# Kernel optimization log

Measured on AMD Instinct MI355X. Metric: run time of the kernel, lower is better.

Reference implementation:

```python
import jax, jax.numpy as jnp
import numpy as np

B, NPG, IN_DIM, H, E = 128, 500, 3, 128, 512000
N = B * NPG
NEG = -1e9  # stands in for -inf masked fill; exp underflows to exactly 0 in fp32
BN_EPS = 1e-5


def setup_inputs() -> dict:
    key = jax.random.key(0)
    ks = jax.random.split(key, 40)
    rn = lambda k, shape: (jax.random.normal(k, shape, jnp.float32) * 0.05)
    x = jax.random.normal(ks[0], (N, IN_DIM), jnp.float32)
    g = jax.random.randint(ks[1], (E,), 0, B)
    src = jax.random.randint(ks[2], (E,), 0, NPG) + g * NPG
    dst = jax.random.randint(ks[3], (E,), 0, NPG) + g * NPG
    edge_index = jnp.stack([src, dst]).astype(jnp.int32)
    batch = (jnp.arange(N) // NPG).astype(jnp.int32)
    feasible_mask = jax.random.uniform(ks[4], (B, NPG, NPG)) < 0.1
    feasible_mask = feasible_mask.at[:, 0, 0].set(True)  # >=1 feasible action/graph
    return dict(
        x=x, edge_index=edge_index, batch=batch, feasible_mask=feasible_mask,
        gin_W1_0=rn(ks[5], (IN_DIM, H)), gin_b1_0=jnp.zeros((H,), jnp.float32),
        gin_g_0=jnp.ones((H,), jnp.float32), gin_be_0=jnp.zeros((H,), jnp.float32),
        gin_W2_0=rn(ks[6], (H, H)), gin_b2_0=jnp.zeros((H,), jnp.float32),
        gin_W1=rn(ks[7], (3, H, H)), gin_b1=jnp.zeros((3, H), jnp.float32),
        gin_g=jnp.ones((3, H), jnp.float32), gin_be=jnp.zeros((3, H), jnp.float32),
        gin_W2=rn(ks[8], (3, H, H)), gin_b2=jnp.zeros((3, H), jnp.float32),
        pol_W1_0=rn(ks[9], (2 * H, H)), pol_b1_0=jnp.zeros((H,), jnp.float32),
        pol_W2_0=rn(ks[10], (H, H)), pol_b2_0=jnp.zeros((H,), jnp.float32),
        pol_W1=rn(ks[11], (2, H, H)), pol_b1=jnp.zeros((2, H), jnp.float32),
        pol_W2=rn(ks[12], (2, H, H)), pol_b2=jnp.zeros((2, H), jnp.float32),
    )


def _gin_conv(h, src, dst, deg, W1, b1, g, be, W2, b2):
    # mean-aggregate neighbors (self loops already in edge list), eps=0
    agg = jax.ops.segment_sum(h[src], dst, num_segments=N) / deg[:, None]
    z = (h + agg) @ W1 + b1
    mu = jnp.mean(z, axis=0)
    var = jnp.var(z, axis=0)  # biased var, as torch BN training mode
    z = (z - mu) * jax.lax.rsqrt(var + BN_EPS) * g + be
    return jax.nn.relu(z) @ W2 + b2


def reference(x, edge_index, batch, feasible_mask,
              gin_W1_0, gin_b1_0, gin_g_0, gin_be_0, gin_W2_0, gin_b2_0,
              gin_W1, gin_b1, gin_g, gin_be, gin_W2, gin_b2,
              pol_W1_0, pol_b1_0, pol_W2_0, pol_b2_0,
              pol_W1, pol_b1, pol_W2, pol_b2):
    # add self loops
    loop = jnp.arange(N, dtype=edge_index.dtype)
    src = jnp.concatenate([edge_index[0], loop])
    dst = jnp.concatenate([edge_index[1], loop])
    deg = jnp.maximum(jax.ops.segment_sum(jnp.ones_like(src, jnp.float32), dst, num_segments=N), 1.0)

    h = _gin_conv(x, src, dst, deg, gin_W1_0, gin_b1_0, gin_g_0, gin_be_0, gin_W2_0, gin_b2_0)
    node_pool = h
    graph_pool = jax.ops.segment_sum(h, batch, num_segments=B) / NPG
    for l in range(3):
        h = _gin_conv(h, src, dst, deg, gin_W1[l], gin_b1[l], gin_g[l], gin_be[l], gin_W2[l], gin_b2[l])
        node_pool = node_pool + h
        graph_pool = graph_pool + jax.ops.segment_sum(h, batch, num_segments=B) / NPG

    # augment node embeds with their graph embed (graphs contiguous, equal size)
    a = jnp.concatenate([node_pool, graph_pool[batch]], axis=-1).reshape(B, NPG, 2 * H)
    a = jnp.tanh(a @ pol_W1_0 + pol_b1_0) @ pol_W2_0 + pol_b2_0
    for l in range(2):
        a = jnp.tanh(a @ pol_W1[l] + pol_b1[l]) @ pol_W2[l] + pol_b2[l]

    scores = jnp.einsum('bnd,bmd->bnm', a, a)                 # [B, n, n]
    scores = jnp.where(feasible_mask, scores, NEG)
    flat = scores.reshape(B, NPG * NPG)
    logp_all = jax.nn.log_softmax(flat, axis=-1)
    actions_id = jax.random.categorical(jax.random.key(42), flat, axis=-1)  # [B]
    log_prob = jnp.take_along_axis(logp_all, actions_id[:, None], axis=1)[:, 0]
    return actions_id, log_prob
```

## Files before the change

kernel.cpp:

```cpp
#include <hip/hip_runtime.h>
#include <float.h>

#define NN 64000
#define BB 128
#define NPGc 500
#define EE 512000

#define SKW(c) ((c) + (((c)>>3)<<2))
#define LW 188

__device__ __forceinline__ unsigned rotl32(unsigned x, unsigned r){ return (x<<r)|(x>>(32u-r)); }

__device__ __forceinline__ unsigned threefry_bits(unsigned idx){
  unsigned x0 = 0u, x1 = idx;
  const unsigned ks0 = 0u, ks1 = 42u, ks2 = 0u ^ 42u ^ 0x1BD11BDAu;
  x0 += ks0; x1 += ks1;
#define RND(r) { x0 += x1; x1 = rotl32(x1, r); x1 ^= x0; }
  RND(13u) RND(15u) RND(26u) RND(6u)   x0 += ks1; x1 += ks2 + 1u;
  RND(17u) RND(29u) RND(16u) RND(24u)  x0 += ks2; x1 += ks0 + 2u;
  RND(13u) RND(15u) RND(26u) RND(6u)   x0 += ks0; x1 += ks1 + 3u;
  RND(17u) RND(29u) RND(16u) RND(24u)  x0 += ks1; x1 += ks2 + 4u;
  RND(13u) RND(15u) RND(26u) RND(6u)   x0 += ks2; x1 += ks0 + 5u;
#undef RND
  return x0 ^ x1;
}

__device__ __forceinline__ float gumbel_of(unsigned idx){
  unsigned bits = threefry_bits(idx);
  float f = __uint_as_float((bits >> 9) | 0x3f800000u) - 1.0f;
  const float TINY = 1.17549435e-38f;
  float u = fmaxf(TINY, f + TINY);
  return -logf(-logf(u));
}

__device__ __forceinline__ float fast_tanh(float x){
  return 1.0f - 2.0f/(__expf(2.0f*x) + 1.0f);
}

__global__ __launch_bounds__(256)
void maskprep_kernel(const unsigned char* __restrict__ mu8src, const int* __restrict__ mi32src,
                     unsigned char* __restrict__ mn8, unsigned char* __restrict__ mt8){
  __shared__ unsigned char tile[64][65];
  const int b = blockIdx.y;
  const int rt = blockIdx.x >> 3, ct = blockIdx.x & 7;
  const int t = threadIdx.x;
  const int lane = t & 63, rr = t >> 6;
  int mybad = (((const unsigned*)mi32src)[t] > 1u) ? 1 : 0;
  int isbool = __syncthreads_or(mybad);
#pragma unroll
  for (int p=0;p<16;p++){
    int row = rt*64 + p*4 + rr;
    int col = ct*64 + lane;
    unsigned char v = 0;
    if (row < NPGc && col < NPGc){
      size_t off = (size_t)b*250000 + (size_t)row*500 + col;
      v = isbool ? mu8src[off] : (unsigned char)(mi32src[off] != 0);
      mn8[off] = v;
    }
    tile[p*4+rr][lane] = v;
  }
  __syncthreads();
#pragma unroll
  for (int p=0;p<16;p++){
    int orow = ct*64 + p*4 + rr;
    int ocol = rt*64 + lane;
    if (orow < NPGc && ocol < NPGc){
      size_t off = (size_t)b*250000 + (size_t)orow*500 + ocol;
      mt8[off] = tile[lane][p*4+rr];
    }
  }
}

__global__ void count_kernel(const int* __restrict__ dst, int* __restrict__ cnt){
  int e = blockIdx.x*256 + threadIdx.x;
  if (e < EE) atomicAdd(&cnt[dst[e]], 1);
}

__global__ void scanA_kernel(const int* __restrict__ cnt, int* __restrict__ bsum){
  __shared__ int red[256];
  int t = threadIdx.x;
  red[t] = cnt[blockIdx.x*256 + t];
  __syncthreads();
  for (int s=128;s>0;s>>=1){
    if (t < s) red[t] += red[t+s];
    __syncthreads();
  }
  if (t == 0) bsum[blockIdx.x] = red[0];
}

__global__ void scanB_kernel(const int* __restrict__ bsum, int* __restrict__ boff){
  __shared__ int red[256];
  int t = threadIdx.x;
  int v = (t < 250) ? bsum[t] : 0;
  red[t] = v;
  __syncthreads();
  for (int d=1; d<256; d<<=1){
    int x = (t >= d) ? red[t-d] : 0;
    __syncthreads();
    red[t] += x;
    __syncthreads();
  }
  if (t < 250) boff[t] = red[t] - v;
  if (t == 249) boff[250] = red[t];
}

__global__ void scanC_kernel(const int* __restrict__ cnt, const int* __restrict__ boff,
                             int* __restrict__ off, int* __restrict__ cur){
  __shared__ int red[256];
  int t = threadIdx.x;
  int n = blockIdx.x*256 + t;
  int v = cnt[n];
  red[t] = v;
  __syncthreads();
  for (int d=1; d<256; d<<=1){
    int x = (t >= d) ? red[t-d] : 0;
    __syncthreads();
    red[t] += x;
    __syncthreads();
  }
  int excl = red[t] - v + boff[blockIdx.x];
  off[n] = excl; cur[n] = excl;
  if (n == NN-1) off[NN] = excl + v;
}

__global__ void fill_kernel(const int* __restrict__ src, const int* __restrict__ dst,
                            int* __restrict__ cur, int* __restrict__ csr){
  int e = blockIdx.x*256 + threadIdx.x;
  if (e < EE){
    int d = dst[e];
    int p = atomicAdd(&cur[d], 1);
    csr[p] = src[e];
  }
}

__global__ __launch_bounds__(256)
void agg128_kernel(const float* __restrict__ h, const int* __restrict__ off,
                   const int* __restrict__ csr, const int* __restrict__ cnt,
                   float* __restrict__ xin){
  const int nb = gridDim.x;
  const int per = nb >> 3;
  int bid = (blockIdx.x % 8)*per + (blockIdx.x >> 3);
  int w = (bid*256 + (int)threadIdx.x) >> 6;
  int lane = threadIdx.x & 63;
  if (w >= NN) return;
  const float* hn = h + (size_t)w*128;
  float a0 = hn[lane], a1 = hn[lane+64];
  float s0 = a0, s1 = a1;
  int e0 = off[w], e1 = off[w+1];
  int e = e0;
  for (; e + 4 <= e1; e += 4){
    int sA = csr[e], sB = csr[e+1], sC = csr[e+2], sD = csr[e+3];
    const float* pA = h + (size_t)sA*128;
    const float* pB = h + (size_t)sB*128;
    const float* pC = h + (size_t)sC*128;
    const float* pD = h + (size_t)sD*128;
    float a0A = pA[lane], a1A = pA[lane+64];
    float a0B = pB[lane], a1B = pB[lane+64];
    float a0C = pC[lane], a1C = pC[lane+64];
    float a0D = pD[lane], a1D = pD[lane+64];
    s0 += a0A; s1 += a1A;
    s0 += a0B; s1 += a1B;
    s0 += a0C; s1 += a1C;
    s0 += a0D; s1 += a1D;
  }
  for (; e < e1; ++e){
    int s = csr[e];
    const float* hs = h + (size_t)s*128;
    s0 += hs[lane]; s1 += hs[lane+64];
  }
  float di = 1.0f/(float)(cnt[w]+1);
  xin[(size_t)w*128 + lane]      = a0 + s0*di;
  xin[(size_t)w*128 + lane + 64] = a1 + s1*di;
}

__global__ __launch_bounds__(256)
void z0_kernel(const float* __restrict__ x, const int* __restrict__ off,
               const int* __restrict__ csr, const int* __restrict__ cnt,
               const float* __restrict__ W, const float* __restrict__ bias,
               float* __restrict__ z, float* __restrict__ stats){
  __shared__ float xr[192];
  __shared__ float ssum[128], ssq[128];
  int t = threadIdx.x;
  int row0 = blockIdx.x*64;
  if (t < 192){
    int nl = t/3, f = t - nl*3;
    int n = row0 + nl;
    float a = x[n*3+f];
    float s = a;
    int e1 = off[n+1];
    for (int e = off[n]; e < e1; ++e) s += x[csr[e]*3 + f];
    float di = 1.0f/(float)(cnt[n]+1);
    xr[t] = a + s*di;
  }
  if (t < 128){ ssum[t]=0.f; ssq[t]=0.f; }
  int f = t & 127, rg = t >> 7;
  float w0 = W[f], w1 = W[128+f], w2 = W[256+f], bb = bias[f];
  __syncthreads();
  float s = 0.f, q = 0.f;
  for (int i=0;i<32;i++){
    int r = rg*32 + i;
    float y = bb + xr[r*3]*w0 + xr[r*3+1]*w1 + xr[r*3+2]*w2;
    z[(size_t)(row0+r)*128 + f] = y;
    s += y; q += y*y;
  }
  atomicAdd(&ssum[f], s); atomicAdd(&ssq[f], q);
  __syncthreads();
  if (t < 128){ atomicAdd(&stats[t], ssum[t]); atomicAdd(&stats[128+t], ssq[t]); }
}

template<int K, bool CATF, bool BNF, bool TANHF, bool STATSF, int POOLM>
__global__ __launch_bounds__(256, 2)
void linear_kernel(const float* X, const float* __restrict__ X2,
                   const float* __restrict__ W, const float* __restrict__ bias,
                   float* Y,
                   const float* __restrict__ statsIn, const float* __restrict__ gam,
                   const float* __restrict__ bet,
                   float* __restrict__ statsOut, float* __restrict__ pool){
  __shared__ __align__(16) float xs[32][LW];
  __shared__ __align__(16) float ws[32][LW];
  __shared__ float ssum[128], ssq[128];
  __shared__ __align__(16) float bnsc_s[128], bnsh_s[128];
  const int t = threadIdx.x;
  const int row0 = blockIdx.x*128;
  const int cg = t & 15, rg = t >> 4;
  const int c0 = cg*8, r0 = rg*8;
  const int skr0 = SKW(r0), skc0 = SKW(c0);
  float acc[8][8];
#pragma unroll
  for (int r=0;r<8;r++)
#pragma unroll
    for (int c=0;c<8;c++) acc[r][c]=0.f;
  if (STATSF && t < 128){ ssum[t]=0.f; ssq[t]=0.f; }
  if (BNF && t < 128){
    float mu  = statsIn[t]     * (1.0f/NN);
    float var = statsIn[128+t] * (1.0f/NN) - mu*mu;
    float rsv = rsqrtf(var + 1e-5f);
    float sc  = gam[t]*rsv;
    bnsc_s[t] = sc;
    bnsh_s[t] = bet[t] - mu*sc;
  }

  for (int kc=0; kc<K; kc+=32){
    __syncthreads();
#pragma unroll
    for (int i=0;i<4;i++){
      int task = t + 256*i;
      int n = task >> 3, k4 = task & 7;
      int gk = kc + k4*4;
      int row = row0 + n;
      float4 v;
      if (CATF){
        if (gk < 128) v = *(const float4*)(X  + (size_t)row*128 + gk);
        else          v = *(const float4*)(X2 + (size_t)(row/NPGc)*128 + (gk-128));
      } else {
        v = *(const float4*)(X + (size_t)row*K + gk);
      }
      if (BNF){
        float4 sc4 = *(const float4*)(bnsc_s + gk);
        float4 sh4 = *(const float4*)(bnsh_s + gk);
        v.x = fmaxf(0.f, v.x*sc4.x + sh4.x);
        v.y = fmaxf(0.f, v.y*sc4.y + sh4.y);
        v.z = fmaxf(0.f, v.z*sc4.z + sh4.z);
        v.w = fmaxf(0.f, v.w*sc4.w + sh4.w);
      }
      int ns = SKW(n);
      xs[k4*4+0][ns] = v.x; xs[k4*4+1][ns] = v.y;
      xs[k4*4+2][ns] = v.z; xs[k4*4+3][ns] = v.w;
    }
#pragma unroll
    for (int i=0;i<4;i++){
      int task = t + 256*i;
      int k = task >> 5, c4 = task & 31;
      float4 v = *(const float4*)(W + (size_t)(kc+k)*128 + c4*4);
      *(float4*)&ws[k][c4*4 + ((c4>>1)<<2)] = v;
    }
    __syncthreads();
#pragma unroll
    for (int k=0;k<32;k++){
      float4 xa = *(const float4*)&xs[k][skr0];
      float4 xb = *(const float4*)&xs[k][skr0+4];
      float4 wa = *(const float4*)&ws[k][skc0];
      float4 wb = *(const float4*)&ws[k][skc0+4];
      float xv[8] = {xa.x,xa.y,xa.z,xa.w,xb.x,xb.y,xb.z,xb.w};
      float wv[8] = {wa.x,wa.y,wa.z,wa.w,wb.x,wb.y,wb.z,wb.w};
#pragma unroll
      for (int r=0;r<8;r++)
#pragma unroll
        for (int c=0;c<8;c++)
          acc[r][c] += xv[r]*wv[c];
    }
  }
  float4 ba = *(const float4*)(bias + c0);
  float4 bb2 = *(const float4*)(bias + c0 + 4);
  float bv[8] = {ba.x,ba.y,ba.z,ba.w,bb2.x,bb2.y,bb2.z,bb2.w};
  float sc8[8], sq8[8];
#pragma unroll
  for (int c=0;c<8;c++){ sc8[c]=0.f; sq8[c]=0.f; }
#pragma unroll
  for (int r=0;r<8;r++){
    int n = row0 + r0 + r;
    float y[8];
#pragma unroll
    for (int c=0;c<8;c++){
      float v = acc[r][c] + bv[c];
      if (TANHF) v = fast_tanh(v);
      y[c] = v;
    }
    float4 y0; y0.x=y[0]; y0.y=y[1]; y0.z=y[2]; y0.w=y[3];
    float4 y1; y1.x=y[4]; y1.y=y[5]; y1.z=y[6]; y1.w=y[7];
    *(float4*)(Y + (size_t)n*128 + c0)     = y0;
    *(float4*)(Y + (size_t)n*128 + c0 + 4) = y1;
    if (POOLM == 1){
      *(float4*)(pool + (size_t)n*128 + c0)     = y0;
      *(float4*)(pool + (size_t)n*128 + c0 + 4) = y1;
    } else if (POOLM == 2){
      float4 p0 = *(const float4*)(pool + (size_t)n*128 + c0);
      float4 p1 = *(const float4*)(pool + (size_t)n*128 + c0 + 4);
      p0.x+=y[0]; p0.y+=y[1]; p0.z+=y[2]; p0.w+=y[3];
      p1.x+=y[4]; p1.y+=y[5]; p1.z+=y[6]; p1.w+=y[7];
      *(float4*)(pool + (size_t)n*128 + c0)     = p0;
      *(float4*)(pool + (size_t)n*128 + c0 + 4) = p1;
    }
    if (STATSF){
#pragma unroll
      for (int c=0;c<8;c++){ sc8[c]+=y[c]; sq8[c]+=y[c]*y[c]; }
    }
  }
  if (STATSF){
#pragma unroll
    for (int c=0;c<8;c++){
      atomicAdd(&ssum[c0+c], sc8[c]);
      atomicAdd(&ssq[c0+c],  sq8[c]);
    }
    __syncthreads();
    if (t < 128){
      atomicAdd(&statsOut[t],     ssum[t]);
      atomicAdd(&statsOut[128+t], ssq[t]);
    }
  }
}

__global__ __launch_bounds__(512)
void gpool_kernel(const float* __restrict__ pool, float* __restrict__ gpool){
  __shared__ float red[4][128];
  int b = blockIdx.x;
  int f = threadIdx.x & 127, part = threadIdx.x >> 7;
  const float* p = pool + (size_t)b*NPGc*128 + f;
  int rbeg = part*125, rend = rbeg + 125;
  float s = 0.f;
  for (int i=rbeg;i<rend;i++) s += p[(size_t)i*128];
  red[part][f] = s;
  __syncthreads();
  if (part == 0){
    float tot = ((red[0][f] + red[1][f]) + red[2][f]) + red[3][f];
    gpool[(size_t)b*128 + f] = tot * (1.0f/NPGc);
  }
}

#define QCAP 1024
#define NPAIR 36

__global__ __launch_bounds__(256)
void scores_tri_kernel(const float* __restrict__ A, const unsigned char* __restrict__ mn8,
                       const unsigned char* __restrict__ mt8, float* __restrict__ partials){
  __shared__ __align__(16) float as[128][68];
  __shared__ __align__(16) float bs[32][68];
  __shared__ float qs[QCAP];
  __shared__ int   qi[QCAP];
  __shared__ int   qcnt;
  float* rm  = qs;
  float* rs_ = qs + 256;
  float* rv  = qs + 512;
  float* rsc = qs + 768;
  int*   ri  = qi;
  const int t = threadIdx.x;
  const int xcd = blockIdx.x & 7;
  const int within = blockIdx.x >> 3;
  const int b = xcd*16 + within/NPAIR;
  int pidx = within % NPAIR, tn = 0;
  while (pidx >= 8 - tn){ pidx -= 8 - tn; tn++; }
  const int tm = tn + pidx;
  const int pair = within % NPAIR;
  const bool diag = (tn == tm);
  const int n0 = tn*64, m0 = tm*64;
  const int cgc = t & 15, rgc = t >> 4;
  const int r0_ = rgc*4, c0 = cgc*4;
  const float* Ab = A + (size_t)b*NPGc*128;
  const unsigned gbase = (unsigned)b*250000u;
  if (t == 0) qcnt = 0;

#pragma unroll
  for (int i=0;i<32;i++){
    int idx = t + 256*i;
    int k = idx & 127, r = idx >> 7;
    int n = n0 + r;
    as[k][r] = (n < NPGc) ? Ab[(size_t)n*128 + k] : 0.f;
  }

  float acc[4][4];
#pragma unroll
  for (int i2=0;i2<4;i2++)
#pragma unroll
    for (int j=0;j<4;j++) acc[i2][j]=0.f;

  for (int kc=0;kc<4;kc++){
    __syncthreads();
#pragma unroll
    for (int i=0;i<8;i++){
      int idx = t + 256*i;
      int kk = idx & 31, c = idx >> 5;
      int m = m0 + c;
      bs[kk][c] = (m < NPGc) ? Ab[(size_t)m*128 + kc*32 + kk] : 0.f;
    }
    __syncthreads();
#pragma unroll
    for (int kk=0;kk<32;kk++){
      float4 av = *(const float4*)&as[kc*32+kk][r0_];
      float4 bv4 = *(const float4*)&bs[kk][c0];
      float a_[4] = {av.x,av.y,av.z,av.w};
      float b_[4] = {bv4.x,bv4.y,bv4.z,bv4.w};
#pragma unroll
      for (int i2=0;i2<4;i2++)
#pragma unroll
        for (int j=0;j<4;j++)
          acc[i2][j] += a_[i2]*b_[j];
    }
  }

  float mrun = -1e30f, srun = 0.f, bval = -FLT_MAX, bsc = 0.f;
  int bidx = 0x7FFFFFFF;
  const int mbase = m0 + c0;
  const bool colok = (mbase < NPGc);
#pragma unroll
  for (int i2=0;i2<4;i2++){
    int n = n0 + r0_ + i2;
    bool rowok = colok && (n < NPGc);
    bool fn[4] = {false,false,false,false};
    bool fm[4] = {false,false,false,false};
    if (rowok){
      size_t moff = (size_t)b*250000 + (size_t)n*500 + (size_t)mbase;
      uchar4 mk = *(const uchar4*)(mn8 + moff);
      fn[0]=mk.x!=0; fn[1]=mk.y!=0; fn[2]=mk.z!=0; fn[3]=mk.w!=0;
      uchar4 tk = *(const uchar4*)(mt8 + moff);
      fm[0]=tk.x!=0; fm[1]=tk.y!=0; fm[2]=tk.z!=0; fm[3]=tk.w!=0;
    }
    float cntj[4], sj[4];
    bool pn[4], pm[4];
#pragma unroll
    for (int j=0;j<4;j++){
      int m = mbase + j;
      bool mok = rowok && (m < NPGc);
      bool keep = mok && (!diag || m >= n);
      bool isde = (n == m);
      float cnt = 0.f; bool a1=false, a2=false;
      if (keep){
        if (isde){ cnt = fn[j] ? 1.f : 0.f; a1 = fn[j]; }
        else { cnt = (fn[j]?1.f:0.f) + (fm[j]?1.f:0.f); a1 = fn[j]; a2 = fm[j]; }
      }
      cntj[j]=cnt; pn[j]=a1; pm[j]=a2;
      sj[j] = (cnt > 0.f) ? acc[i2][j] : -1e30f;
    }
    float tmx = fmaxf(fmaxf(sj[0],sj[1]), fmaxf(sj[2],sj[3]));
    float nm = fmaxf(mrun, tmx);
    float add = 0.f;
#pragma unroll
    for (int j=0;j<4;j++) add += cntj[j]*__expf(sj[j] - nm);
    srun = srun*__expf(mrun - nm) + add;
    mrun = nm;
#pragma unroll
    for (int j=0;j<4;j++){
      int m = mbase + j;
      if (pn[j] || pm[j]){
        float s = acc[i2][j];
#pragma unroll
        for (int d=0;d<2;d++){
          bool doit = d ? pm[j] : pn[j];
          if (doit){
            int lidx = d ? (m*500 + n) : (n*500 + m);
            int slot = atomicAdd(&qcnt, 1);
            if (slot < QCAP){ qs[slot] = s; qi[slot] = lidx; }
            else {
              float g = gumbel_of(gbase + (unsigned)lidx);
              float val = s + g;
              if (val > bval || (val == bval && lidx < bidx)){ bval = val; bidx = lidx; bsc = s; }
            }
          }
        }
      }
    }
  }
  __syncthreads();
  int qn = qcnt; if (qn > QCAP) qn = QCAP;
  for (int i = t; i < qn; i += 256){
    float s = qs[i]; int idx = qi[i];
    float g = gumbel_of(gbase + (unsigned)idx);
    float val = s + g;
    if (val > bval || (val == bval && idx < bidx)){ bval = val; bidx = idx; bsc = s; }
  }
  __syncthreads();
  rm[t]=mrun; rs_[t]=srun; rv[t]=bval; ri[t]=bidx; rsc[t]=bsc;
  __syncthreads();
  for (int offr=128; offr>0; offr>>=1){
    if (t < offr){
      float m1 = rm[t], s1 = rs_[t];
      float m2 = rm[t+offr], s2 = rs_[t+offr];
      float M = fmaxf(m1, m2);
      float S = s1*expf(m1-M) + s2*expf(m2-M);
      rm[t] = M; rs_[t] = S;
      float v2 = rv[t+offr]; int i2_ = ri[t+offr];
      if (v2 > rv[t] || (v2 == rv[t] && i2_ < ri[t])){ rv[t]=v2; ri[t]=i2_; rsc[t]=rsc[t+offr]; }
    }
    __syncthreads();
  }
  if (t == 0){
    float* p = partials + ((size_t)b*NPAIR + pair)*8;
    p[0]=rm[0]; p[1]=rs_[0]; p[2]=rv[0]; p[3]=(float)ri[0]; p[4]=rsc[0];
  }
}

__global__ void finalize_kernel(const float* __restrict__ partials, float* __restrict__ out){
  int b = threadIdx.x;
  float M = -1e30f, S = 0.f, BV = -FLT_MAX, BS = 0.f;
  int BI = 0x7FFFFFFF;
  for (int tp=0; tp<NPAIR; tp++){
    const float* p = partials + ((size_t)b*NPAIR + tp)*8;
    float m = p[0], s = p[1], v = p[2]; int i = (int)p[3]; float sc2 = p[4];
    float nM = fmaxf(M, m);
    S = S*expf(M-nM) + s*expf(m-nM);
    M = nM;
    if (v > BV || (v == BV && i < BI)){ BV = v; BI = i; BS = sc2; }
  }
  out[b]      = (float)BI;
  out[BB + b] = BS - (M + logf(S));
}

extern "C" void kernel_launch(void* const* d_in, const int* in_sizes, int n_in,
                              void* d_out, int out_size, void* d_ws, size_t ws_size,
                              hipStream_t stream){
  const float* x        = (const float*)d_in[0];
  const int*   eidx     = (const int*)d_in[1];
  const void*  maskp    = d_in[3];
  const float* gin_W1_0 = (const float*)d_in[4];
  const float* gin_b1_0 = (const float*)d_in[5];
  const float* gin_g_0  = (const float*)d_in[6];
  const float* gin_be_0 = (const float*)d_in[7];
  const float* gin_W2_0 = (const float*)d_in[8];
  const float* gin_b2_0 = (const float*)d_in[9];
  const float* gin_W1   = (const float*)d_in[10];
  const float* gin_b1   = (const float*)d_in[11];
  const float* gin_g    = (const float*)d_in[12];
  const float* gin_be   = (const float*)d_in[13];
  const float* gin_W2   = (const float*)d_in[14];
  const float* gin_b2   = (const float*)d_in[15];
  const float* pol_W1_0 = (const float*)d_in[16];
  const float* pol_b1_0 = (const float*)d_in[17];
  const float* pol_W2_0 = (const float*)d_in[18];
  const float* pol_b2_0 = (const float*)d_in[19];
  const float* pol_W1   = (const float*)d_in[20];
  const float* pol_b1   = (const float*)d_in[21];
  const float* pol_W2   = (const float*)d_in[22];
  const float* pol_b2   = (const float*)d_in[23];
  float* out = (float*)d_out;

  char* p = (char*)d_ws;
  auto carve = [&](size_t bytes) -> void* {
    void* r = (void*)p; p += (bytes + 255) & ~(size_t)255; return r;
  };
  float* hbuf  = (float*)carve((size_t)NN*128*4);
  float* xin   = (float*)carve((size_t)NN*128*4);
  float* pool  = (float*)carve((size_t)NN*128*4);
  float* gpool = (float*)carve((size_t)BB*128*4);
  float* stats = (float*)carve(4*256*4);
  float* partials = (float*)carve((size_t)BB*NPAIR*8*4);
  int* cnt  = (int*)carve((size_t)NN*4);
  int* off  = (int*)carve((size_t)(NN+1)*4);
  int* cur  = (int*)carve((size_t)NN*4);
  int* csr  = (int*)carve((size_t)EE*4);
  int* bsum = (int*)carve(256*4);
  int* boff = (int*)carve(256*4);
  unsigned char* mn8 = (unsigned char*)carve((size_t)BB*250000);
  unsigned char* mt8 = (unsigned char*)carve((size_t)BB*250000);

  const int* srcp = eidx;
  const int* dstp = eidx + EE;

  {
    dim3 mg(64, BB);
    maskprep_kernel<<<mg, 256, 0, stream>>>((const unsigned char*)maskp, (const int*)maskp,
                                            mn8, mt8);
  }

  hipMemsetAsync(cnt, 0, (size_t)NN*4, stream);
  hipMemsetAsync(stats, 0, 4*256*4, stream);
  count_kernel<<<(EE+255)/256, 256, 0, stream>>>(dstp, cnt);
  scanA_kernel<<<NN/256, 256, 0, stream>>>(cnt, bsum);
  scanB_kernel<<<1, 256, 0, stream>>>(bsum, boff);
  scanC_kernel<<<NN/256, 256, 0, stream>>>(cnt, boff, off, cur);
  fill_kernel<<<(EE+255)/256, 256, 0, stream>>>(srcp, dstp, cur, csr);

  z0_kernel<<<NN/64, 256, 0, stream>>>(x, off, csr, cnt, gin_W1_0, gin_b1_0, xin, stats);
  linear_kernel<128,false,true,false,false,1><<<NN/128, 256, 0, stream>>>(
      xin, nullptr, gin_W2_0, gin_b2_0, hbuf, stats, gin_g_0, gin_be_0, nullptr, pool);

  for (int l=0; l<3; l++){
    float* st = stats + (l+1)*256;
    agg128_kernel<<<NN/4, 256, 0, stream>>>(hbuf, off, csr, cnt, xin);
    linear_kernel<128,false,false,false,true,0><<<NN/128, 256, 0, stream>>>(
        xin, nullptr, gin_W1 + (size_t)l*16384, gin_b1 + l*128, xin,
        nullptr, nullptr, nullptr, st, nullptr);
    linear_kernel<128,false,true,false,false,2><<<NN/128, 256, 0, stream>>>(
        xin, nullptr, gin_W2 + (size_t)l*16384, gin_b2 + l*128, hbuf,
        st, gin_g + l*128, gin_be + l*128, nullptr, pool);
  }

  gpool_kernel<<<BB, 512, 0, stream>>>(pool, gpool);
  linear_kernel<256,true,false,true,false,0><<<NN/128, 256, 0, stream>>>(
      pool, gpool, pol_W1_0, pol_b1_0, hbuf, nullptr, nullptr, nullptr, nullptr, nullptr);
  linear_kernel<128,false,false,false,false,0><<<NN/128, 256, 0, stream>>>(
      hbuf, nullptr, pol_W2_0, pol_b2_0, xin, nullptr, nullptr, nullptr, nullptr, nullptr);
  linear_kernel<128,false,false,true,false,0><<<NN/128, 256, 0, stream>>>(
      xin, nullptr, pol_W1, pol_b1, hbuf, nullptr, nullptr, nullptr, nullptr, nullptr);
  linear_kernel<128,false,false,false,false,0><<<NN/128, 256, 0, stream>>>(
      hbuf, nullptr, pol_W2, pol_b2, xin, nullptr, nullptr, nullptr, nullptr, nullptr);
  linear_kernel<128,false,false,true,false,0><<<NN/128, 256, 0, stream>>>(
      xin, nullptr, pol_W1 + 16384, pol_b1 + 128, hbuf, nullptr, nullptr, nullptr, nullptr, nullptr);
  linear_kernel<128,false,false,false,false,0><<<NN/128, 256, 0, stream>>>(
      hbuf, nullptr, pol_W2 + 16384, pol_b2 + 128, xin, nullptr, nullptr, nullptr, nullptr, nullptr);

  scores_tri_kernel<<<8*16*NPAIR, 256, 0, stream>>>(xin, mn8, mt8, partials);
  finalize_kernel<<<1, BB, 0, stream>>>(partials, out);
}
```

Measured before the change: 1.206 ms.

## Fuse neighbor aggregation with first GIN linear layer and vectorize mask prep

Replaces the separate aggregation kernel and the first GIN linear kernel with one fused kernel. It aggregates 64 rows into padded shared memory, multiplies them by W1 staged in shared memory, and accumulates the BN statistics. This removes the write and reread of the aggregated features in global memory, at the cost of a different gather pattern (4 threads per node with float4 loads) and more shared memory per block. The mask prep kernel also switches to 4-byte vector loads and stores.

```diff
diff --git a/kernel.cpp b/kernel.cpp
--- a/kernel.cpp
+++ b/kernel.cpp
@@ -8,6 +8,7 @@
 
 #define SKW(c) ((c) + (((c)>>3)<<2))
 #define LW 188
+#define TSTR 144
 
 __device__ __forceinline__ unsigned rotl32(unsigned x, unsigned r){ return (x<<r)|(x>>(32u-r)); }
 
@@ -44,29 +45,41 @@
   const int b = blockIdx.y;
   const int rt = blockIdx.x >> 3, ct = blockIdx.x & 7;
   const int t = threadIdx.x;
-  const int lane = t & 63, rr = t >> 6;
   int mybad = (((const unsigned*)mi32src)[t] > 1u) ? 1 : 0;
   int isbool = __syncthreads_or(mybad);
-#pragma unroll
-  for (int p=0;p<16;p++){
-    int row = rt*64 + p*4 + rr;
-    int col = ct*64 + lane;
-    unsigned char v = 0;
+  const int rl = t >> 4;
+  const int cq = t & 15;
+#pragma unroll
+  for (int p=0;p<4;p++){
+    int row = rt*64 + p*16 + rl;
+    int col = ct*64 + cq*4;
+    uchar4 v; v.x=0; v.y=0; v.z=0; v.w=0;
     if (row < NPGc && col < NPGc){
-      size_t off = (size_t)b*250000 + (size_t)row*500 + col;
-      v = isbool ? mu8src[off] : (unsigned char)(mi32src[off] != 0);
-      mn8[off] = v;
-    }
-    tile[p*4+rr][lane] = v;
-  }
-  __syncthreads();
-#pragma unroll
-  for (int p=0;p<16;p++){
-    int orow = ct*64 + p*4 + rr;
-    int ocol = rt*64 + lane;
+      size_t o = (size_t)b*250000 + (size_t)row*500 + col;
+      if (isbool){
+        v = *(const uchar4*)(mu8src + o);
+      } else {
+        int4 w = *(const int4*)(mi32src + o);
+        v.x = (unsigned char)(w.x!=0); v.y = (unsigned char)(w.y!=0);
+        v.z = (unsigned char)(w.z!=0); v.w = (unsigned char)(w.w!=0);
+      }
+      *(uchar4*)(mn8 + o) = v;
+    }
+    int lr = p*16 + rl, lc = cq*4;
+    tile[lr][lc+0]=v.x; tile[lr][lc+1]=v.y; tile[lr][lc+2]=v.z; tile[lr][lc+3]=v.w;
+  }
+  __syncthreads();
+#pragma unroll
+  for (int p=0;p<4;p++){
+    int orow = ct*64 + p*16 + rl;
+    int ocol = rt*64 + cq*4;
     if (orow < NPGc && ocol < NPGc){
-      size_t off = (size_t)b*250000 + (size_t)orow*500 + ocol;
-      mt8[off] = tile[lane][p*4+rr];
+      uchar4 v;
+      v.x = tile[cq*4+0][p*16+rl];
+      v.y = tile[cq*4+1][p*16+rl];
+      v.z = tile[cq*4+2][p*16+rl];
+      v.w = tile[cq*4+3][p*16+rl];
+      *(uchar4*)(mt8 + (size_t)b*250000 + (size_t)orow*500 + ocol) = v;
     }
   }
 }
@@ -133,44 +146,149 @@
   }
 }
 
-__global__ __launch_bounds__(256)
-void agg128_kernel(const float* __restrict__ h, const int* __restrict__ off,
-                   const int* __restrict__ csr, const int* __restrict__ cnt,
-                   float* __restrict__ xin){
-  const int nb = gridDim.x;
-  const int per = nb >> 3;
-  int bid = (blockIdx.x % 8)*per + (blockIdx.x >> 3);
-  int w = (bid*256 + (int)threadIdx.x) >> 6;
-  int lane = threadIdx.x & 63;
-  if (w >= NN) return;
-  const float* hn = h + (size_t)w*128;
-  float a0 = hn[lane], a1 = hn[lane+64];
-  float s0 = a0, s1 = a1;
-  int e0 = off[w], e1 = off[w+1];
-  int e = e0;
-  for (; e + 4 <= e1; e += 4){
-    int sA = csr[e], sB = csr[e+1], sC = csr[e+2], sD = csr[e+3];
-    const float* pA = h + (size_t)sA*128;
-    const float* pB = h + (size_t)sB*128;
-    const float* pC = h + (size_t)sC*128;
-    const float* pD = h + (size_t)sD*128;
-    float a0A = pA[lane], a1A = pA[lane+64];
-    float a0B = pB[lane], a1B = pB[lane+64];
-    float a0C = pC[lane], a1C = pC[lane+64];
-    float a0D = pD[lane], a1D = pD[lane+64];
-    s0 += a0A; s1 += a1A;
-    s0 += a0B; s1 += a1B;
-    s0 += a0C; s1 += a1C;
-    s0 += a0D; s1 += a1D;
-  }
-  for (; e < e1; ++e){
-    int s = csr[e];
-    const float* hs = h + (size_t)s*128;
-    s0 += hs[lane]; s1 += hs[lane+64];
-  }
-  float di = 1.0f/(float)(cnt[w]+1);
-  xin[(size_t)w*128 + lane]      = a0 + s0*di;
-  xin[(size_t)w*128 + lane + 64] = a1 + s1*di;
+__global__ __launch_bounds__(256, 2)
+void aggz_kernel(const float* __restrict__ h, const int* __restrict__ off,
+                 const int* __restrict__ csr, const int* __restrict__ cnt,
+                 const float* __restrict__ W, const float* __restrict__ bias,
+                 float* __restrict__ Y, float* __restrict__ statsOut){
+  __shared__ __align__(16) float tmp[64*TSTR + 64];
+  __shared__ __align__(16) float ws2[4672];
+  __shared__ float ssum[128], ssq[128];
+  const int t = threadIdx.x;
+  int bid = ((blockIdx.x & 7) << 7) + (blockIdx.x >> 3);
+  if (bid >= 1000) return;
+  const int row0 = bid*64;
+  if (t < 128){ ssum[t]=0.f; ssq[t]=0.f; }
+
+  {
+    const int rl = t >> 2;
+    const int f0 = (t & 3) * 32;
+    const int n = row0 + rl;
+    const float* hb = h + (size_t)n*128 + f0;
+    float a[32], s[32];
+#pragma unroll
+    for (int i=0;i<8;i++){
+      float4 v = *(const float4*)(hb + i*4);
+      a[i*4+0]=v.x; a[i*4+1]=v.y; a[i*4+2]=v.z; a[i*4+3]=v.w;
+    }
+#pragma unroll
+    for (int f=0;f<32;f++) s[f] = a[f];
+    int e0 = off[n], e1 = off[n+1];
+    int e = e0;
+    for (; e+2 <= e1; e += 2){
+      int sA = csr[e], sB = csr[e+1];
+      const float* pA = h + (size_t)sA*128 + f0;
+      const float* pB = h + (size_t)sB*128 + f0;
+      float vA[32], vB[32];
+#pragma unroll
+      for (int i=0;i<8;i++){
+        float4 va = *(const float4*)(pA + i*4);
+        float4 vb = *(const float4*)(pB + i*4);
+        vA[i*4+0]=va.x; vA[i*4+1]=va.y; vA[i*4+2]=va.z; vA[i*4+3]=va.w;
+        vB[i*4+0]=vb.x; vB[i*4+1]=vb.y; vB[i*4+2]=vb.z; vB[i*4+3]=vb.w;
+      }
+#pragma unroll
+      for (int f=0;f<32;f++){ s[f] += vA[f]; s[f] += vB[f]; }
+    }
+    for (; e < e1; ++e){
+      const float* pA = h + (size_t)csr[e]*128 + f0;
+      float vA[32];
+#pragma unroll
+      for (int i=0;i<8;i++){
+        float4 va = *(const float4*)(pA + i*4);
+        vA[i*4+0]=va.x; vA[i*4+1]=va.y; vA[i*4+2]=va.z; vA[i*4+3]=va.w;
+      }
+#pragma unroll
+      for (int f=0;f<32;f++) s[f] += vA[f];
+    }
+    float di = 1.0f/(float)(cnt[n]+1);
+    int base = rl*TSTR + ((rl>>3)<<2) + f0 + ((f0>>5)<<2);
+#pragma unroll
+    for (int i=0;i<8;i++){
+      float4 v;
+      v.x = a[i*4+0] + s[i*4+0]*di;
+      v.y = a[i*4+1] + s[i*4+1]*di;
+      v.z = a[i*4+2] + s[i*4+2]*di;
+      v.w = a[i*4+3] + s[i*4+3]*di;
+      *(float4*)&tmp[base + i*4] = v;
+    }
+  }
+
+  const int cg = t & 15, rg = t >> 4;
+  const int c0 = cg*8, r0 = rg*4;
+  float acc[4][8];
+#pragma unroll
+  for (int r=0;r<4;r++)
+#pragma unroll
+    for (int c=0;c<8;c++) acc[r][c]=0.f;
+
+  for (int kc=0; kc<128; kc+=32){
+    __syncthreads();
+#pragma unroll
+    for (int i=0;i<4;i++){
+      int task = t + 256*i;
+      int k = task >> 5, cq = task & 31;
+      float4 v = *(const float4*)(W + (size_t)(kc+k)*128 + cq*4);
+      int c = cq*4;
+      ws2[(c+0)*36 + (((c+0)>>3)<<2) + k] = v.x;
+      ws2[(c+1)*36 + (((c+1)>>3)<<2) + k] = v.y;
+      ws2[(c+2)*36 + (((c+2)>>3)<<2) + k] = v.z;
+      ws2[(c+3)*36 + (((c+3)>>3)<<2) + k] = v.w;
+    }
+    __syncthreads();
+#pragma unroll
+    for (int k4=0;k4<8;k4++){
+      int kk = kc + k4*4;
+      int koff = kk + ((kk>>5)<<2);
+      float4 xr[4];
+#pragma unroll
+      for (int r=0;r<4;r++)
+        xr[r] = *(const float4*)&tmp[(r0+r)*TSTR + (((r0+r)>>3)<<2) + koff];
+      float4 wc[8];
+#pragma unroll
+      for (int c=0;c<8;c++)
+        wc[c] = *(const float4*)&ws2[(c0+c)*36 + (((c0+c)>>3)<<2) + k4*4];
+#pragma unroll
+      for (int r=0;r<4;r++)
+#pragma unroll
+        for (int c=0;c<8;c++){
+          acc[r][c] += xr[r].x*wc[c].x;
+          acc[r][c] += xr[r].y*wc[c].y;
+          acc[r][c] += xr[r].z*wc[c].z;
+          acc[r][c] += xr[r].w*wc[c].w;
+        }
+    }
+  }
+  float4 ba = *(const float4*)(bias + c0);
+  float4 bb2 = *(const float4*)(bias + c0 + 4);
+  float bv[8] = {ba.x,ba.y,ba.z,ba.w,bb2.x,bb2.y,bb2.z,bb2.w};
+  float sc8[8], sq8[8];
+#pragma unroll
+  for (int c=0;c<8;c++){ sc8[c]=0.f; sq8[c]=0.f; }
+#pragma unroll
+  for (int r=0;r<4;r++){
+    int n = row0 + r0 + r;
+    float y[8];
+#pragma unroll
+    for (int c=0;c<8;c++){
+      y[c] = acc[r][c] + bv[c];
+      sc8[c] += y[c]; sq8[c] += y[c]*y[c];
+    }
+    float4 y0; y0.x=y[0]; y0.y=y[1]; y0.z=y[2]; y0.w=y[3];
+    float4 y1; y1.x=y[4]; y1.y=y[5]; y1.z=y[6]; y1.w=y[7];
+    *(float4*)(Y + (size_t)n*128 + c0)     = y0;
+    *(float4*)(Y + (size_t)n*128 + c0 + 4) = y1;
+  }
+#pragma unroll
+  for (int c=0;c<8;c++){
+    atomicAdd(&ssum[c0+c], sc8[c]);
+    atomicAdd(&ssq[c0+c],  sq8[c]);
+  }
+  __syncthreads();
+  if (t < 128){
+    atomicAdd(&statsOut[t],     ssum[t]);
+    atomicAdd(&statsOut[128+t], ssq[t]);
+  }
 }
 
 __global__ __launch_bounds__(256)
@@ -604,10 +722,8 @@
 
   for (int l=0; l<3; l++){
     float* st = stats + (l+1)*256;
-    agg128_kernel<<<NN/4, 256, 0, stream>>>(hbuf, off, csr, cnt, xin);
-    linear_kernel<128,false,false,false,true,0><<<NN/128, 256, 0, stream>>>(
-        xin, nullptr, gin_W1 + (size_t)l*16384, gin_b1 + l*128, xin,
-        nullptr, nullptr, nullptr, st, nullptr);
+    aggz_kernel<<<1024, 256, 0, stream>>>(hbuf, off, csr, cnt,
+        gin_W1 + (size_t)l*16384, gin_b1 + l*128, xin, st);
     linear_kernel<128,false,true,false,false,2><<<NN/128, 256, 0, stream>>>(
         xin, nullptr, gin_W2 + (size_t)l*16384, gin_b2 + l*128, hbuf,
         st, gin_g + l*128, gin_be + l*128, nullptr, pool);
```

Result: slower. 1.286 ms (+6.7%).
